# Kernel tuning notes

Hardware: AMD Instinct MI355X
Metric: run time of the kernel (lower is better)

The kernel has to match this reference:

```python
import jax, jax.numpy as jnp
import numpy as np

N_NODES = 50000
N_EDGES = 640000
N_REL = 8
IN_DIM = 128
HID_DIM = 128
OUT_DIM = 64


def setup_inputs() -> dict:
    key = jax.random.key(0)
    ks = jax.random.split(key, 8)
    features = jax.random.normal(ks[0], (N_NODES, IN_DIM), dtype=jnp.float32)
    src = jax.random.randint(ks[1], (N_EDGES,), 0, N_NODES, dtype=jnp.int32)
    dst = jax.random.randint(ks[2], (N_EDGES,), 0, N_NODES, dtype=jnp.int32)
    edge_types = jax.random.randint(ks[3], (N_EDGES,), 0, N_REL, dtype=jnp.int32)
    s1 = 1.0 / np.sqrt(IN_DIM)
    s2 = 1.0 / np.sqrt(HID_DIM)
    W1 = jax.random.normal(ks[4], (N_REL, IN_DIM, HID_DIM), dtype=jnp.float32) * s1
    W1_self = jax.random.normal(ks[5], (IN_DIM, HID_DIM), dtype=jnp.float32) * s1
    b1 = jnp.zeros((HID_DIM,), dtype=jnp.float32)
    W2 = jax.random.normal(ks[6], (N_REL, HID_DIM, OUT_DIM), dtype=jnp.float32) * s2
    W2_self = jax.random.normal(ks[7], (HID_DIM, OUT_DIM), dtype=jnp.float32) * s2
    b2 = jnp.zeros((OUT_DIM,), dtype=jnp.float32)
    return {"features": features, "src": src, "dst": dst, "edge_types": edge_types,
            "W1": W1, "W1_self": W1_self, "b1": b1,
            "W2": W2, "W2_self": W2_self, "b2": b2}


def _rel_graph_conv(h, src, dst, edge_types, W, W_self, b):
    # Precompute relation-specific transforms for all nodes: [R, N, Dout]
    rel = jnp.einsum('nd,rdo->rno', h, W)
    # Gather per-edge message W[etype(e)] @ h[src(e)]: [E, Dout]
    msg = rel[edge_types, src]
    # Scatter-sum to destination nodes
    agg = jax.ops.segment_sum(msg, dst, num_segments=h.shape[0])
    # Self-loop + bias (DGL RelGraphConv defaults: self_loop=True, bias=True)
    return agg + h @ W_self + b


def reference(features, src, dst, edge_types, W1, W1_self, b1, W2, W2_self, b2):
    h = jax.nn.relu(_rel_graph_conv(features, src, dst, edge_types, W1, W1_self, b1))
    logits = _rel_graph_conv(h, src, dst, edge_types, W2, W2_self, b2)
    return logits
```

## Files before the change

kernel.cpp:

```cpp
#include <hip/hip_runtime.h>
#include <hip/hip_bf16.h>
#include <stdint.h>

#define NN 50000
#define NE 640000
#define NR 8
#define NB_SCAN ((NN + 1023) / 1024)

typedef short bf16x8 __attribute__((ext_vector_type(8)));
typedef float f32x4  __attribute__((ext_vector_type(4)));

__device__ __forceinline__ unsigned short f2bf(float f) {
    union { float f; unsigned u; } v; v.f = f;
    unsigned r = v.u + 0x7FFF + ((v.u >> 16) & 1);
    return (unsigned short)(r >> 16);
}
__device__ __forceinline__ float bf2f(unsigned short s) {
    union { unsigned u; float f; } v; v.u = ((unsigned)s) << 16; return v.f;
}

__global__ void hist_kernel(const int* __restrict__ dst, int* __restrict__ counts) {
    int e = blockIdx.x * 256 + threadIdx.x;
    if (e < NE) atomicAdd(&counts[dst[e]], 1);
}

__global__ __launch_bounds__(1024) void blocksum_kernel(const int* __restrict__ counts,
                                                        int* __restrict__ bsum) {
    __shared__ int ws[16];
    int i = blockIdx.x * 1024 + threadIdx.x;
    int v = (i < NN) ? counts[i] : 0;
    #pragma unroll
    for (int d = 32; d > 0; d >>= 1) v += __shfl_down(v, d, 64);
    int wid = threadIdx.x >> 6, lane = threadIdx.x & 63;
    if (lane == 0) ws[wid] = v;
    __syncthreads();
    if (threadIdx.x < 16) {
        int s = ws[threadIdx.x];
        #pragma unroll
        for (int d = 8; d > 0; d >>= 1) s += __shfl_down(s, d, 16);
        if (threadIdx.x == 0) bsum[blockIdx.x] = s;
    }
}

__global__ __launch_bounds__(64) void scanbase_kernel(const int* __restrict__ bsum,
                                                      int* __restrict__ base,
                                                      int* __restrict__ offsets) {
    int lane = threadIdx.x;
    int v = (lane < NB_SCAN) ? bsum[lane] : 0;
    int incl = v;
    #pragma unroll
    for (int d = 1; d < 64; d <<= 1) {
        int n = __shfl_up(incl, d, 64);
        if (lane >= d) incl += n;
    }
    if (lane < NB_SCAN) base[lane] = incl - v;
    if (lane == 63) offsets[NN] = incl;
}

__global__ __launch_bounds__(1024) void scanlocal_kernel(const int* __restrict__ counts,
                                                         const int* __restrict__ base,
                                                         int* __restrict__ offsets,
                                                         int* __restrict__ cursor) {
    __shared__ int ws[16];
    __shared__ int wbase[16];
    int t = threadIdx.x;
    int i = blockIdx.x * 1024 + t;
    int v = (i < NN) ? counts[i] : 0;
    int lane = t & 63, wid = t >> 6;
    int incl = v;
    #pragma unroll
    for (int d = 1; d < 64; d <<= 1) {
        int n = __shfl_up(incl, d, 64);
        if (lane >= d) incl += n;
    }
    if (lane == 63) ws[wid] = incl;
    __syncthreads();
    if (t < 16) {
        int s = ws[t];
        int si = s;
        #pragma unroll
        for (int d = 1; d < 16; d <<= 1) {
            int n = __shfl_up(si, d, 16);
            if (t >= d) si += n;
        }
        wbase[t] = si - s;
    }
    __syncthreads();
    if (i < NN) {
        int excl = base[blockIdx.x] + wbase[wid] + incl - v;
        offsets[i] = excl;
        cursor[i]  = excl;
    }
}

__global__ void fill_kernel(const int* __restrict__ src, const int* __restrict__ dst,
                            const int* __restrict__ et, int* __restrict__ cursor,
                            int* __restrict__ rows) {
    int e = blockIdx.x * 256 + threadIdx.x;
    if (e < NE) {
        int pos = atomicAdd(&cursor[dst[e]], 1);
        rows[pos] = et[e] * NN + src[e];
    }
}

__global__ void cvt_bf16_kernel(const float* __restrict__ in, unsigned short* __restrict__ outp,
                                int n8) {
    int i = blockIdx.x * 256 + threadIdx.x;
    if (i >= n8) return;
    const float4* pp = (const float4*)in + (size_t)i * 2;
    float4 a = pp[0], b = pp[1];
    uint4 o;
    o.x = (unsigned)f2bf(a.x) | ((unsigned)f2bf(a.y) << 16);
    o.y = (unsigned)f2bf(a.z) | ((unsigned)f2bf(a.w) << 16);
    o.z = (unsigned)f2bf(b.x) | ((unsigned)f2bf(b.y) << 16);
    o.w = (unsigned)f2bf(b.z) | ((unsigned)f2bf(b.w) << 16);
    ((uint4*)outp)[i] = o;
}

template<int DOUTV>
__global__ void prepW_kernel(const float* __restrict__ W, const float* __restrict__ Wself,
                             unsigned short* __restrict__ WT) {
    int idx = blockIdx.x * 256 + threadIdx.x;
    if (idx >= 9 * DOUTV * 128) return;
    int k = idx & 127;
    int c = idx >> 7;
    int r = c / DOUTV;
    int o = c - r * DOUTV;
    float v = (r < 8) ? W[((size_t)r * 128 + k) * DOUTV + o]
                      : Wself[(size_t)k * DOUTV + o];
    WT[idx] = f2bf(v);
}

template<int BN, int BM>
__global__ __launch_bounds__(256) void mfma_gemm_kernel(
        const unsigned short* __restrict__ A,
        const unsigned short* __restrict__ WT,
        const float*  __restrict__ bias,
        unsigned short* __restrict__ relout,
        float*  __restrict__ selfout,
        int M) {
    __shared__ unsigned short Xs[BM * 128];
    __shared__ unsigned short Ws[BN * 128];
    const int t  = threadIdx.x;
    const int mb = blockIdx.x;
    const int bn = blockIdx.y;

    #pragma unroll
    for (int i = 0; i < BM / 16; i++) {
        int g = t + i * 256;
        int row = g >> 4, c = g & 15;
        int m = mb * BM + row;
        float4 v = make_float4(0.f, 0.f, 0.f, 0.f);
        if (m < M) v = *(const float4*)(A + (size_t)m * 128 + c * 8);
        *(float4*)((char*)Xs + row * 256 + ((c ^ (row & 15)) << 4)) = v;
    }
    #pragma unroll
    for (int i = 0; i < BN / 16; i++) {
        int g = t + i * 256;
        int row = g >> 4, c = g & 15;
        float4 v = *(const float4*)(WT + ((size_t)bn * BN + row) * 128 + c * 8);
        *(float4*)((char*)Ws + row * 256 + ((c ^ (row & 15)) << 4)) = v;
    }
    __syncthreads();

    const int lane = t & 63;
    const int w    = t >> 6;
    const int wm   = (BN == 128) ? (w & 1) * 64 : w * 64;
    const int wn   = (BN == 128) ? (w >> 1) * 64 : 0;
    const int r15  = lane & 15;
    const int q    = lane >> 4;

    f32x4 acc[4][4] = {};
    #pragma unroll
    for (int ks = 0; ks < 4; ks++) {
        bf16x8 af[4], bfr[4];
        int c = (ks * 4 + q) ^ r15;
        #pragma unroll
        for (int i = 0; i < 4; i++) {
            int row = wm + i * 16 + r15;
            af[i] = *(const bf16x8*)((const char*)Xs + row * 256 + (c << 4));
        }
        #pragma unroll
        for (int j = 0; j < 4; j++) {
            int row = wn + j * 16 + r15;
            bfr[j] = *(const bf16x8*)((const char*)Ws + row * 256 + (c << 4));
        }
        #pragma unroll
        for (int i = 0; i < 4; i++)
            #pragma unroll
            for (int j = 0; j < 4; j++)
                acc[i][j] = __builtin_amdgcn_mfma_f32_16x16x32_bf16(af[i], bfr[j], acc[i][j], 0, 0, 0);
    }

    const int rowq = q * 4;
    if (bn < 8) {
        unsigned short* O = relout + (size_t)bn * M * BN;
        #pragma unroll
        for (int i = 0; i < 4; i++) {
            #pragma unroll
            for (int reg = 0; reg < 4; reg++) {
                int m = mb * BM + wm + i * 16 + rowq + reg;
                if (m < M) {
                    #pragma unroll
                    for (int j = 0; j < 4; j++) {
                        int n = wn + j * 16 + r15;
                        O[(size_t)m * BN + n] = f2bf(acc[i][j][reg]);
                    }
                }
            }
        }
    } else {
        #pragma unroll
        for (int j = 0; j < 4; j++) {
            float bv = bias[wn + j * 16 + r15];
            #pragma unroll
            for (int i = 0; i < 4; i++) {
                #pragma unroll
                for (int reg = 0; reg < 4; reg++) {
                    int m = mb * BM + wm + i * 16 + rowq + reg;
                    if (m < M)
                        selfout[(size_t)m * BN + wn + j * 16 + r15] = acc[i][j][reg] + bv;
                }
            }
        }
    }
}

template<int DIM, bool RELU, bool OUTBF16>
__global__ __launch_bounds__(64) void gather_kernel(
        const int* __restrict__ offsets, const int* __restrict__ rows,
        const unsigned short* __restrict__ rel, const float* __restrict__ selfin,
        void* __restrict__ outp) {
    int n = blockIdx.x;
    int t = threadIdx.x;
    int o0 = offsets[n], o1 = offsets[n + 1];
    if (DIM == 128) {
        float2 acc = *(const float2*)&selfin[(size_t)n * 128 + 2 * t];
        for (int j = o0; j < o1; j++) {
            size_t row = (size_t)rows[j];
            unsigned pv = *(const unsigned*)&rel[row * 128 + 2 * t];
            acc.x += bf2f((unsigned short)(pv & 0xffff));
            acc.y += bf2f((unsigned short)(pv >> 16));
        }
        if (RELU) { acc.x = fmaxf(acc.x, 0.f); acc.y = fmaxf(acc.y, 0.f); }
        if (OUTBF16) {
            unsigned pv = (unsigned)f2bf(acc.x) | ((unsigned)f2bf(acc.y) << 16);
            ((unsigned*)outp)[(size_t)n * 64 + t] = pv;
        } else {
            ((float2*)outp)[(size_t)n * 64 + t] = acc;
        }
    } else {
        float acc = selfin[(size_t)n * 64 + t];
        for (int j = o0; j < o1; j++)
            acc += bf2f(rel[(size_t)rows[j] * 64 + t]);
        if (RELU) acc = fmaxf(acc, 0.f);
        ((float*)outp)[(size_t)n * 64 + t] = acc;
    }
}

extern "C" void kernel_launch(void* const* d_in, const int* in_sizes, int n_in,
                              void* d_out, int out_size, void* d_ws, size_t ws_size,
                              hipStream_t stream) {
    const float* X   = (const float*)d_in[0];
    const int*   src = (const int*)d_in[1];
    const int*   dst = (const int*)d_in[2];
    const int*   et  = (const int*)d_in[3];
    const float* W1  = (const float*)d_in[4];
    const float* W1s = (const float*)d_in[5];
    const float* b1  = (const float*)d_in[6];
    const float* W2  = (const float*)d_in[7];
    const float* W2s = (const float*)d_in[8];
    const float* b2  = (const float*)d_in[9];
    float* out = (float*)d_out;

    char* p = (char*)d_ws;
    unsigned short* rel = (unsigned short*)p; p += (size_t)NR * NN * 128 * 2;
    float* hself = (float*)p;          p += (size_t)NN * 128 * 4;
    unsigned short* Xbf = (unsigned short*)p; p += (size_t)NN * 128 * 2;
    unsigned short* W1T = (unsigned short*)p; p += (size_t)9 * 128 * 128 * 2;
    unsigned short* W2T = (unsigned short*)p; p += (size_t)9 * 64 * 128 * 2;
    int* counts  = (int*)p; p += (size_t)NN * 4;
    int* offsets = (int*)p; p += (size_t)(NN + 4) * 4;
    int* cursor  = (int*)p; p += (size_t)NN * 4;
    int* rows    = (int*)p; p += (size_t)NE * 4;
    int* bsum    = (int*)p; p += 64 * 4;
    int* bbase   = (int*)p; p += 64 * 4;

    hipMemsetAsync(counts, 0, NN * sizeof(int), stream);
    hist_kernel<<<(NE + 255) / 256, 256, 0, stream>>>(dst, counts);
    blocksum_kernel<<<NB_SCAN, 1024, 0, stream>>>(counts, bsum);
    scanbase_kernel<<<1, 64, 0, stream>>>(bsum, bbase, offsets);
    scanlocal_kernel<<<NB_SCAN, 1024, 0, stream>>>(counts, bbase, offsets, cursor);
    fill_kernel<<<(NE + 255) / 256, 256, 0, stream>>>(src, dst, et, cursor, rows);

    cvt_bf16_kernel<<<(NN * 128 / 8 + 255) / 256, 256, 0, stream>>>(X, Xbf, NN * 128 / 8);
    prepW_kernel<128><<<(9 * 128 * 128 + 255) / 256, 256, 0, stream>>>(W1, W1s, W1T);
    prepW_kernel<64><<<(9 * 64 * 128 + 255) / 256, 256, 0, stream>>>(W2, W2s, W2T);

    mfma_gemm_kernel<128, 128><<<dim3((NN + 127) / 128, 9), 256, 0, stream>>>(
        Xbf, W1T, b1, rel, hself, NN);
    gather_kernel<128, true, true><<<NN, 64, 0, stream>>>(offsets, rows, rel, hself, Xbf);

    mfma_gemm_kernel<64, 256><<<dim3((NN + 255) / 256, 9), 256, 0, stream>>>(
        Xbf, W2T, b2, rel, out, NN);
    gather_kernel<64, false, false><<<NN, 64, 0, stream>>>(offsets, rows, rel, out, out);
}
```

Measured before the change: 347.5 us.

## Aggregate-then-transform with per-relation CSR and fused gather+MFMA layer kernel

Replaces the transform-then-gather scheme, which materialised eight relation-specific feature matrices per node, with aggregate-first: edges are sorted by (relation, destination). For each 64-node tile, the kernel scatter-adds bf16 source features into an fp32 LDS buffer with shared-memory atomics, converts the result to bf16, and multiplies by that relation's weight using MFMA, all inside a single fused kernel per layer. This removes the large bf16 relation intermediate and its write/read traffic, and merges the self-loop, bias and ReLU into the same kernel. In exchange it adds LDS atomics, weights read straight from global memory inside the MFMA loop, eight serialized relation passes with barriers per block, a larger scan over N*R counts, and extra bf16 rounding of the aggregated sums.

```diff
diff --git a/kernel.cpp b/kernel.cpp
--- a/kernel.cpp
+++ b/kernel.cpp
@@ -5,7 +5,8 @@
 #define NN 50000
 #define NE 640000
 #define NR 8
-#define NB_SCAN ((NN + 1023) / 1024)
+#define NK (NR * NN)
+#define NB2 ((NK + 1023) / 1024)
 
 typedef short bf16x8 __attribute__((ext_vector_type(8)));
 typedef float f32x4  __attribute__((ext_vector_type(4)));
@@ -15,20 +16,18 @@
     unsigned r = v.u + 0x7FFF + ((v.u >> 16) & 1);
     return (unsigned short)(r >> 16);
 }
-__device__ __forceinline__ float bf2f(unsigned short s) {
-    union { unsigned u; float f; } v; v.u = ((unsigned)s) << 16; return v.f;
-}
-
-__global__ void hist_kernel(const int* __restrict__ dst, int* __restrict__ counts) {
+
+__global__ void hist2_kernel(const int* __restrict__ dst, const int* __restrict__ et,
+                             int* __restrict__ counts) {
     int e = blockIdx.x * 256 + threadIdx.x;
-    if (e < NE) atomicAdd(&counts[dst[e]], 1);
+    if (e < NE) atomicAdd(&counts[et[e] * NN + dst[e]], 1);
 }
 
 __global__ __launch_bounds__(1024) void blocksum_kernel(const int* __restrict__ counts,
-                                                        int* __restrict__ bsum) {
+                                                        int* __restrict__ bsum, int n) {
     __shared__ int ws[16];
     int i = blockIdx.x * 1024 + threadIdx.x;
-    int v = (i < NN) ? counts[i] : 0;
+    int v = (i < n) ? counts[i] : 0;
     #pragma unroll
     for (int d = 32; d > 0; d >>= 1) v += __shfl_down(v, d, 64);
     int wid = threadIdx.x >> 6, lane = threadIdx.x & 63;
@@ -42,64 +41,78 @@
     }
 }
 
-__global__ __launch_bounds__(64) void scanbase_kernel(const int* __restrict__ bsum,
-                                                      int* __restrict__ base,
-                                                      int* __restrict__ offsets) {
-    int lane = threadIdx.x;
-    int v = (lane < NB_SCAN) ? bsum[lane] : 0;
+__global__ __launch_bounds__(512) void scanbase_kernel(const int* __restrict__ bsum,
+                                                       int* __restrict__ base,
+                                                       int* __restrict__ total, int nb) {
+    __shared__ int ws[8];
+    int t = threadIdx.x, lane = t & 63, wid = t >> 6;
+    int v = (t < nb) ? bsum[t] : 0;
     int incl = v;
     #pragma unroll
     for (int d = 1; d < 64; d <<= 1) {
-        int n = __shfl_up(incl, d, 64);
-        if (lane >= d) incl += n;
-    }
-    if (lane < NB_SCAN) base[lane] = incl - v;
-    if (lane == 63) offsets[NN] = incl;
+        int nv = __shfl_up(incl, d, 64);
+        if (lane >= d) incl += nv;
+    }
+    if (lane == 63) ws[wid] = incl;
+    __syncthreads();
+    if (t < 8) {
+        int s = ws[t], si = s;
+        #pragma unroll
+        for (int d = 1; d < 8; d <<= 1) {
+            int nv = __shfl_up(si, d, 64);
+            if (t >= d) si += nv;
+        }
+        ws[t] = si - s;
+    }
+    __syncthreads();
+    int excl = ws[wid] + incl - v;
+    if (t < nb) base[t] = excl;
+    if (t == 511) total[0] = ws[7] + incl;
 }
 
 __global__ __launch_bounds__(1024) void scanlocal_kernel(const int* __restrict__ counts,
                                                          const int* __restrict__ base,
                                                          int* __restrict__ offsets,
-                                                         int* __restrict__ cursor) {
+                                                         int* __restrict__ cursor, int n) {
     __shared__ int ws[16];
     __shared__ int wbase[16];
     int t = threadIdx.x;
     int i = blockIdx.x * 1024 + t;
-    int v = (i < NN) ? counts[i] : 0;
+    int v = (i < n) ? counts[i] : 0;
     int lane = t & 63, wid = t >> 6;
     int incl = v;
     #pragma unroll
     for (int d = 1; d < 64; d <<= 1) {
-        int n = __shfl_up(incl, d, 64);
-        if (lane >= d) incl += n;
+        int nv = __shfl_up(incl, d, 64);
+        if (lane >= d) incl += nv;
     }
     if (lane == 63) ws[wid] = incl;
     __syncthreads();
     if (t < 16) {
-        int s = ws[t];
-        int si = s;
+        int s = ws[t], si = s;
         #pragma unroll
         for (int d = 1; d < 16; d <<= 1) {
-            int n = __shfl_up(si, d, 16);
-            if (t >= d) si += n;
+            int nv = __shfl_up(si, d, 16);
+            if (t >= d) si += nv;
         }
         wbase[t] = si - s;
     }
     __syncthreads();
-    if (i < NN) {
+    if (i < n) {
         int excl = base[blockIdx.x] + wbase[wid] + incl - v;
         offsets[i] = excl;
         cursor[i]  = excl;
     }
 }
 
-__global__ void fill_kernel(const int* __restrict__ src, const int* __restrict__ dst,
-                            const int* __restrict__ et, int* __restrict__ cursor,
-                            int* __restrict__ rows) {
+__global__ void fill2_kernel(const int* __restrict__ src, const int* __restrict__ dst,
+                             const int* __restrict__ et, int* __restrict__ cursor,
+                             int* __restrict__ esrc, int* __restrict__ edst) {
     int e = blockIdx.x * 256 + threadIdx.x;
     if (e < NE) {
-        int pos = atomicAdd(&cursor[dst[e]], 1);
-        rows[pos] = et[e] * NN + src[e];
+        int pos = atomicAdd(&cursor[et[e] * NN + dst[e]], 1);
+        esrc[pos] = src[e];
+        edst[pos] = dst[e];
     }
 }
 
@@ -131,130 +144,129 @@
     WT[idx] = f2bf(v);
 }
 
-template<int BN, int BM>
-__global__ __launch_bounds__(256) void mfma_gemm_kernel(
+template<int NOUT, bool RELU, bool OUTBF16>
+__global__ __launch_bounds__(256) void fused_layer(
         const unsigned short* __restrict__ A,
         const unsigned short* __restrict__ WT,
-        const float*  __restrict__ bias,
-        unsigned short* __restrict__ relout,
-        float*  __restrict__ selfout,
-        int M) {
-    __shared__ unsigned short Xs[BM * 128];
-    __shared__ unsigned short Ws[BN * 128];
-    const int t  = threadIdx.x;
-    const int mb = blockIdx.x;
-    const int bn = blockIdx.y;
-
-    #pragma unroll
-    for (int i = 0; i < BM / 16; i++) {
-        int g = t + i * 256;
+        const float* __restrict__ bias,
+        const int* __restrict__ off2,
+        const int* __restrict__ esrc,
+        const int* __restrict__ edst,
+        void* __restrict__ outp, int M) {
+    constexpr int CW = NOUT / 4;
+    constexpr int NJ = CW / 16;
+    __shared__ float Af[64 * 132];
+    __shared__ unsigned short Asw[64 * 128];
+
+    const int t = threadIdx.x;
+    const int n0 = blockIdx.x * 64;
+    const int bm = (M - n0 < 64) ? (M - n0) : 64;
+    const int lane = t & 63;
+    const int w = t >> 6;
+    const int r15 = lane & 15;
+    const int q = lane >> 4;
+
+    f32x4 acc[4][NJ] = {};
+
+    auto do_mfma = [&](int rr) {
+        #pragma unroll
+        for (int ks = 0; ks < 4; ks++) {
+            int c = (ks * 4 + q) ^ r15;
+            bf16x8 af[4];
+            #pragma unroll
+            for (int i = 0; i < 4; i++)
+                af[i] = *(const bf16x8*)((const char*)Asw + (i * 16 + r15) * 256 + (c << 4));
+            #pragma unroll
+            for (int j = 0; j < NJ; j++) {
+                bf16x8 bf = *(const bf16x8*)(WT +
+                    ((size_t)(rr * NOUT + w * CW + j * 16 + r15) << 7) + ks * 32 + q * 8);
+                #pragma unroll
+                for (int i = 0; i < 4; i++)
+                    acc[i][j] = __builtin_amdgcn_mfma_f32_16x16x32_bf16(af[i], bf, acc[i][j], 0, 0, 0);
+            }
+        }
+    };
+
+    #pragma unroll
+    for (int kk = 0; kk < 4; kk++) {
+        int g = t + kk * 256;
         int row = g >> 4, c = g & 15;
-        int m = mb * BM + row;
-        float4 v = make_float4(0.f, 0.f, 0.f, 0.f);
-        if (m < M) v = *(const float4*)(A + (size_t)m * 128 + c * 8);
-        *(float4*)((char*)Xs + row * 256 + ((c ^ (row & 15)) << 4)) = v;
-    }
-    #pragma unroll
-    for (int i = 0; i < BN / 16; i++) {
-        int g = t + i * 256;
-        int row = g >> 4, c = g & 15;
-        float4 v = *(const float4*)(WT + ((size_t)bn * BN + row) * 128 + c * 8);
-        *(float4*)((char*)Ws + row * 256 + ((c ^ (row & 15)) << 4)) = v;
-    }
-    __syncthreads();
-
-    const int lane = t & 63;
-    const int w    = t >> 6;
-    const int wm   = (BN == 128) ? (w & 1) * 64 : w * 64;
-    const int wn   = (BN == 128) ? (w >> 1) * 64 : 0;
-    const int r15  = lane & 15;
-    const int q    = lane >> 4;
-
-    f32x4 acc[4][4] = {};
-    #pragma unroll
-    for (int ks = 0; ks < 4; ks++) {
-        bf16x8 af[4], bfr[4];
-        int c = (ks * 4 + q) ^ r15;
+        uint4 v = make_uint4(0, 0, 0, 0);
+        if (row < bm) v = *(const uint4*)(A + ((size_t)(n0 + row) << 7) + c * 8);
+        *(uint4*)((char*)Asw + row * 256 + ((c ^ (row & 15)) << 4)) = v;
+    }
+    __syncthreads();
+    do_mfma(8);
+
+    for (int r = 0; r < 8; r++) {
+        #pragma unroll
+        for (int z = 0; z < 9; z++) {
+            int s4 = t + z * 256;
+            if (s4 < 2112) ((float4*)Af)[s4] = make_float4(0.f, 0.f, 0.f, 0.f);
+        }
+        __syncthreads();
+
+        int e0 = off2[r * NN + n0];
+        int e1 = off2[r * NN + n0 + bm];
+        for (int eb = e0 + w * 4; eb < e1; eb += 16) {
+            int ne = e1 - eb; ne = (ne > 4) ? 4 : ne;
+            int ss[4], dd[4];
+            #pragma unroll
+            for (int i = 0; i < 4; i++)
+                if (i < ne) { ss[i] = esrc[eb + i]; dd[i] = edst[eb + i] - n0; }
+            unsigned vv[4];
+            #pragma unroll
+            for (int i = 0; i < 4; i++)
+                if (i < ne) vv[i] = ((const unsigned*)A)[((size_t)ss[i] << 6) + lane];
+            #pragma unroll
+            for (int i = 0; i < 4; i++)
+                if (i < ne) {
+                    atomicAdd(&Af[dd[i] * 132 + lane],      __uint_as_float(vv[i] << 16));
+                    atomicAdd(&Af[dd[i] * 132 + 66 + lane], __uint_as_float(vv[i] & 0xffff0000u));
+                }
+        }
+        __syncthreads();
+
+        #pragma unroll
+        for (int kk = 0; kk < 4; kk++) {
+            int g = t + kk * 256;
+            int row = g >> 4, cc = g & 15;
+            const float* rp = &Af[row * 132];
+            unsigned short tmp[8];
+            #pragma unroll
+            for (int j = 0; j < 8; j++)
+                tmp[j] = f2bf(rp[(j & 1) * 66 + cc * 4 + (j >> 1)]);
+            uint4 pv;
+            pv.x = (unsigned)tmp[0] | ((unsigned)tmp[1] << 16);
+            pv.y = (unsigned)tmp[2] | ((unsigned)tmp[3] << 16);
+            pv.z = (unsigned)tmp[4] | ((unsigned)tmp[5] << 16);
+            pv.w = (unsigned)tmp[6] | ((unsigned)tmp[7] << 16);
+            *(uint4*)((char*)Asw + row * 256 + ((cc ^ (row & 15)) << 4)) = pv;
+        }
+        __syncthreads();
+
+        do_mfma(r);
+    }
+
+    #pragma unroll
+    for (int j = 0; j < NJ; j++) {
+        int col = w * CW + j * 16 + r15;
+        float bv = bias[col];
         #pragma unroll
         for (int i = 0; i < 4; i++) {
-            int row = wm + i * 16 + r15;
-            af[i] = *(const bf16x8*)((const char*)Xs + row * 256 + (c << 4));
-        }
-        #pragma unroll
-        for (int j = 0; j < 4; j++) {
-            int row = wn + j * 16 + r15;
-            bfr[j] = *(const bf16x8*)((const char*)Ws + row * 256 + (c << 4));
-        }
-        #pragma unroll
-        for (int i = 0; i < 4; i++)
-            #pragma unroll
-            for (int j = 0; j < 4; j++)
-                acc[i][j] = __builtin_amdgcn_mfma_f32_16x16x32_bf16(af[i], bfr[j], acc[i][j], 0, 0, 0);
-    }
-
-    const int rowq = q * 4;
-    if (bn < 8) {
-        unsigned short* O = relout + (size_t)bn * M * BN;
-        #pragma unroll
-        for (int i = 0; i < 4; i++) {
             #pragma unroll
             for (int reg = 0; reg < 4; reg++) {
-                int m = mb * BM + wm + i * 16 + rowq + reg;
+                int m = n0 + i * 16 + q * 4 + reg;
                 if (m < M) {
-                    #pragma unroll
-                    for (int j = 0; j < 4; j++) {
-                        int n = wn + j * 16 + r15;
-                        O[(size_t)m * BN + n] = f2bf(acc[i][j][reg]);
-                    }
+                    float v = acc[i][j][reg] + bv;
+                    if (RELU) v = fmaxf(v, 0.f);
+                    if (OUTBF16)
+                        ((unsigned short*)outp)[(size_t)m * NOUT + col] = f2bf(v);
+                    else
+                        ((float*)outp)[(size_t)m * NOUT + col] = v;
                 }
             }
         }
-    } else {
-        #pragma unroll
-        for (int j = 0; j < 4; j++) {
-            float bv = bias[wn + j * 16 + r15];
-            #pragma unroll
-            for (int i = 0; i < 4; i++) {
-                #pragma unroll
-                for (int reg = 0; reg < 4; reg++) {
-                    int m = mb * BM + wm + i * 16 + rowq + reg;
-                    if (m < M)
-                        selfout[(size_t)m * BN + wn + j * 16 + r15] = acc[i][j][reg] + bv;
-                }
-            }
-        }
-    }
-}
-
-template<int DIM, bool RELU, bool OUTBF16>
-__global__ __launch_bounds__(64) void gather_kernel(
-        const int* __restrict__ offsets, const int* __restrict__ rows,
-        const unsigned short* __restrict__ rel, const float* __restrict__ selfin,
-        void* __restrict__ outp) {
-    int n = blockIdx.x;
-    int t = threadIdx.x;
-    int o0 = offsets[n], o1 = offsets[n + 1];
-    if (DIM == 128) {
-        float2 acc = *(const float2*)&selfin[(size_t)n * 128 + 2 * t];
-        for (int j = o0; j < o1; j++) {
-            size_t row = (size_t)rows[j];
-            unsigned pv = *(const unsigned*)&rel[row * 128 + 2 * t];
-            acc.x += bf2f((unsigned short)(pv & 0xffff));
-            acc.y += bf2f((unsigned short)(pv >> 16));
-        }
-        if (RELU) { acc.x = fmaxf(acc.x, 0.f); acc.y = fmaxf(acc.y, 0.f); }
-        if (OUTBF16) {
-            unsigned pv = (unsigned)f2bf(acc.x) | ((unsigned)f2bf(acc.y) << 16);
-            ((unsigned*)outp)[(size_t)n * 64 + t] = pv;
-        } else {
-            ((float2*)outp)[(size_t)n * 64 + t] = acc;
-        }
-    } else {
-        float acc = selfin[(size_t)n * 64 + t];
-        for (int j = o0; j < o1; j++)
-            acc += bf2f(rel[(size_t)rows[j] * 64 + t]);
-        if (RELU) acc = fmaxf(acc, 0.f);
-        ((float*)outp)[(size_t)n * 64 + t] = acc;
     }
 }
 
@@ -274,34 +286,33 @@
     float* out = (float*)d_out;
 
     char* p = (char*)d_ws;
-    unsigned short* rel = (unsigned short*)p; p += (size_t)NR * NN * 128 * 2;
-    float* hself = (float*)p;          p += (size_t)NN * 128 * 4;
     unsigned short* Xbf = (unsigned short*)p; p += (size_t)NN * 128 * 2;
+    unsigned short* hbf = (unsigned short*)p; p += (size_t)NN * 128 * 2;
     unsigned short* W1T = (unsigned short*)p; p += (size_t)9 * 128 * 128 * 2;
     unsigned short* W2T = (unsigned short*)p; p += (size_t)9 * 64 * 128 * 2;
-    int* counts  = (int*)p; p += (size_t)NN * 4;
-    int* offsets = (int*)p; p += (size_t)(NN + 4) * 4;
-    int* cursor  = (int*)p; p += (size_t)NN * 4;
-    int* rows    = (int*)p; p += (size_t)NE * 4;
-    int* bsum    = (int*)p; p += 64 * 4;
-    int* bbase   = (int*)p; p += 64 * 4;
-
-    hipMemsetAsync(counts, 0, NN * sizeof(int), stream);
-    hist_kernel<<<(NE + 255) / 256, 256, 0, stream>>>(dst, counts);
-    blocksum_kernel<<<NB_SCAN, 1024, 0, stream>>>(counts, bsum);
-    scanbase_kernel<<<1, 64, 0, stream>>>(bsum, bbase, offsets);
-    scanlocal_kernel<<<NB_SCAN, 1024, 0, stream>>>(counts, bbase, offsets, cursor);
-    fill_kernel<<<(NE + 255) / 256, 256, 0, stream>>>(src, dst, et, cursor, rows);
+    int* counts2 = (int*)p; p += (size_t)NK * 4;
+    int* off2    = (int*)p; p += (size_t)(NK + 4) * 4;
+    int* cursor2 = (int*)p; p += (size_t)NK * 4;
+    int* esrc    = (int*)p; p += (size_t)NE * 4;
+    int* edst    = (int*)p; p += (size_t)NE * 4;
+    int* bsum    = (int*)p; p += 512 * 4;
+    int* bbase   = (int*)p; p += 512 * 4;
+
+    hipMemsetAsync(counts2, 0, (size_t)NK * sizeof(int), stream);
+    hist2_kernel<<<(NE + 255) / 256, 256, 0, stream>>>(dst, et, counts2);
+    blocksum_kernel<<<NB2, 1024, 0, stream>>>(counts2, bsum, NK);
+    scanbase_kernel<<<1, 512, 0, stream>>>(bsum, bbase, &off2[NK], NB2);
+    scanlocal_kernel<<<NB2, 1024, 0, stream>>>(counts2, bbase, off2, cursor2, NK);
+    fill2_kernel<<<(NE + 255) / 256, 256, 0, stream>>>(src, dst, et, cursor2, esrc, edst);
 
     cvt_bf16_kernel<<<(NN * 128 / 8 + 255) / 256, 256, 0, stream>>>(X, Xbf, NN * 128 / 8);
     prepW_kernel<128><<<(9 * 128 * 128 + 255) / 256, 256, 0, stream>>>(W1, W1s, W1T);
     prepW_kernel<64><<<(9 * 64 * 128 + 255) / 256, 256, 0, stream>>>(W2, W2s, W2T);
 
-    mfma_gemm_kernel<128, 128><<<dim3((NN + 127) / 128, 9), 256, 0, stream>>>(
-        Xbf, W1T, b1, rel, hself, NN);
-    gather_kernel<128, true, true><<<NN, 64, 0, stream>>>(offsets, rows, rel, hself, Xbf);
-
-    mfma_gemm_kernel<64, 256><<<dim3((NN + 255) / 256, 9), 256, 0, stream>>>(
-        Xbf, W2T, b2, rel, out, NN);
-    gather_kernel<64, false, false><<<NN, 64, 0, stream>>>(offsets, rows, rel, out, out);
-}
+    const int nblk = (NN + 63) / 64;
+
+    fused_layer<128, true, true><<<nblk, 256, 0, stream>>>(
+        Xbf, W1T, b1, off2, esrc, edst, hbf, NN);
+    fused_layer<64, false, false><<<nblk, 256, 0, stream>>>(
+        hbf, W2T, b2, off2, esrc, edst, out, NN);
+}
```

After: 1.331 ms. 283% more time.

## Read GEMM weights directly from global, pack gathers four nodes per block

Applied to the files above, without the earlier changes.

The GEMM no longer stages the weight tile in shared memory. Each wave loads its B fragments straight from global or L2, which halves LDS use and may raise occupancy, and layer 2 now uses 128-row tiles. The gather kernels process four destination nodes per 256-thread block and unroll the edge loop by four, so more row loads are in flight. The scan base kernel is generalised to 512 threads, which adds some overhead in exchange for flexibility.

```diff
diff --git a/kernel.cpp b/kernel.cpp
--- a/kernel.cpp
+++ b/kernel.cpp
@@ -5,7 +5,7 @@
 #define NN 50000
 #define NE 640000
 #define NR 8
-#define NB_SCAN ((NN + 1023) / 1024)
+#define NB1 ((NN + 1023) / 1024)
 
 typedef short bf16x8 __attribute__((ext_vector_type(8)));
 typedef float f32x4  __attribute__((ext_vector_type(4)));
@@ -25,10 +25,10 @@
 }
 
 __global__ __launch_bounds__(1024) void blocksum_kernel(const int* __restrict__ counts,
-                                                        int* __restrict__ bsum) {
+                                                        int* __restrict__ bsum, int n) {
     __shared__ int ws[16];
     int i = blockIdx.x * 1024 + threadIdx.x;
-    int v = (i < NN) ? counts[i] : 0;
+    int v = (i < n) ? counts[i] : 0;
     #pragma unroll
     for (int d = 32; d > 0; d >>= 1) v += __shfl_down(v, d, 64);
     int wid = threadIdx.x >> 6, lane = threadIdx.x & 63;
@@ -42,51 +42,64 @@
     }
 }
 
-__global__ __launch_bounds__(64) void scanbase_kernel(const int* __restrict__ bsum,
-                                                      int* __restrict__ base,
-                                                      int* __restrict__ offsets) {
-    int lane = threadIdx.x;
-    int v = (lane < NB_SCAN) ? bsum[lane] : 0;
+__global__ __launch_bounds__(512) void scanbase_kernel(const int* __restrict__ bsum,
+                                                       int* __restrict__ base,
+                                                       int* __restrict__ total, int nb) {
+    __shared__ int ws[8];
+    int t = threadIdx.x, lane = t & 63, wid = t >> 6;
+    int v = (t < nb) ? bsum[t] : 0;
     int incl = v;
     #pragma unroll
     for (int d = 1; d < 64; d <<= 1) {
-        int n = __shfl_up(incl, d, 64);
-        if (lane >= d) incl += n;
-    }
-    if (lane < NB_SCAN) base[lane] = incl - v;
-    if (lane == 63) offsets[NN] = incl;
+        int nv = __shfl_up(incl, d, 64);
+        if (lane >= d) incl += nv;
+    }
+    if (lane == 63) ws[wid] = incl;
+    __syncthreads();
+    if (t < 8) {
+        int s = ws[t], si = s;
+        #pragma unroll
+        for (int d = 1; d < 8; d <<= 1) {
+            int nv = __shfl_up(si, d, 64);
+            if (t >= d) si += nv;
+        }
+        ws[t] = si - s;
+    }
+    __syncthreads();
+    int excl = ws[wid] + incl - v;
+    if (t < nb) base[t] = excl;
+    if (t == 511) total[0] = ws[7] + incl;
 }
 
 __global__ __launch_bounds__(1024) void scanlocal_kernel(const int* __restrict__ counts,
                                                          const int* __restrict__ base,
                                                          int* __restrict__ offsets,
-                                                         int* __restrict__ cursor) {
+                                                         int* __restrict__ cursor, int n) {
     __shared__ int ws[16];
     __shared__ int wbase[16];
     int t = threadIdx.x;
     int i = blockIdx.x * 1024 + t;
-    int v = (i < NN) ? counts[i] : 0;
+    int v = (i < n) ? counts[i] : 0;
     int lane = t & 63, wid = t >> 6;
     int incl = v;
     #pragma unroll
     for (int d = 1; d < 64; d <<= 1) {
-        int n = __shfl_up(incl, d, 64);
-        if (lane >= d) incl += n;
+        int nv = __shfl_up(incl, d, 64);
+        if (lane >= d) incl += nv;
     }
     if (lane == 63) ws[wid] = incl;
     __syncthreads();
     if (t < 16) {
-        int s = ws[t];
-        int si = s;
+        int s = ws[t], si = s;
         #pragma unroll
         for (int d = 1; d < 16; d <<= 1) {
-            int n = __shfl_up(si, d, 16);
-            if (t >= d) si += n;
+            int nv = __shfl_up(si, d, 16);
+            if (t >= d) si += nv;
         }
         wbase[t] = si - s;
     }
     __syncthreads();
-    if (i < NN) {
+    if (i < n) {
         int excl = base[blockIdx.x] + wbase[wid] + incl - v;
         offsets[i] = excl;
         cursor[i]  = excl;
@@ -131,131 +144,138 @@
     WT[idx] = f2bf(v);
 }
 
-template<int BN, int BM>
-__global__ __launch_bounds__(256) void mfma_gemm_kernel(
+template<int NOUT>
+__global__ __launch_bounds__(256) void gemm_split(
         const unsigned short* __restrict__ A,
         const unsigned short* __restrict__ WT,
         const float*  __restrict__ bias,
         unsigned short* __restrict__ relout,
         float*  __restrict__ selfout,
         int M) {
-    __shared__ unsigned short Xs[BM * 128];
-    __shared__ unsigned short Ws[BN * 128];
+    constexpr int NJ = NOUT / 32;
+    __shared__ unsigned short Xs[128 * 128];
     const int t  = threadIdx.x;
     const int mb = blockIdx.x;
     const int bn = blockIdx.y;
 
     #pragma unroll
-    for (int i = 0; i < BM / 16; i++) {
+    for (int i = 0; i < 8; i++) {
         int g = t + i * 256;
         int row = g >> 4, c = g & 15;
-        int m = mb * BM + row;
-        float4 v = make_float4(0.f, 0.f, 0.f, 0.f);
-        if (m < M) v = *(const float4*)(A + (size_t)m * 128 + c * 8);
-        *(float4*)((char*)Xs + row * 256 + ((c ^ (row & 15)) << 4)) = v;
-    }
-    #pragma unroll
-    for (int i = 0; i < BN / 16; i++) {
-        int g = t + i * 256;
-        int row = g >> 4, c = g & 15;
-        float4 v = *(const float4*)(WT + ((size_t)bn * BN + row) * 128 + c * 8);
-        *(float4*)((char*)Ws + row * 256 + ((c ^ (row & 15)) << 4)) = v;
+        int m = mb * 128 + row;
+        uint4 v = make_uint4(0, 0, 0, 0);
+        if (m < M) v = *(const uint4*)(A + ((size_t)m << 7) + c * 8);
+        *(uint4*)((char*)Xs + row * 256 + ((c ^ (row & 15)) << 4)) = v;
     }
     __syncthreads();
 
     const int lane = t & 63;
     const int w    = t >> 6;
-    const int wm   = (BN == 128) ? (w & 1) * 64 : w * 64;
-    const int wn   = (BN == 128) ? (w >> 1) * 64 : 0;
+    const int wm   = (w & 1) * 64;
+    const int wn   = (w >> 1) * (NOUT / 2);
     const int r15  = lane & 15;
     const int q    = lane >> 4;
 
-    f32x4 acc[4][4] = {};
+    f32x4 acc[4][NJ] = {};
     #pragma unroll
     for (int ks = 0; ks < 4; ks++) {
-        bf16x8 af[4], bfr[4];
         int c = (ks * 4 + q) ^ r15;
-        #pragma unroll
-        for (int i = 0; i < 4; i++) {
-            int row = wm + i * 16 + r15;
-            af[i] = *(const bf16x8*)((const char*)Xs + row * 256 + (c << 4));
-        }
-        #pragma unroll
-        for (int j = 0; j < 4; j++) {
-            int row = wn + j * 16 + r15;
-            bfr[j] = *(const bf16x8*)((const char*)Ws + row * 256 + (c << 4));
-        }
+        bf16x8 af[4];
         #pragma unroll
         for (int i = 0; i < 4; i++)
+            af[i] = *(const bf16x8*)((const char*)Xs + (wm + i * 16 + r15) * 256 + (c << 4));
+        #pragma unroll
+        for (int j = 0; j < NJ; j++) {
+            bf16x8 bf = *(const bf16x8*)(WT +
+                ((size_t)(bn * NOUT + wn + j * 16 + r15) << 7) + ks * 32 + q * 8);
             #pragma unroll
-            for (int j = 0; j < 4; j++)
-                acc[i][j] = __builtin_amdgcn_mfma_f32_16x16x32_bf16(af[i], bfr[j], acc[i][j], 0, 0, 0);
+            for (int i = 0; i < 4; i++)
+                acc[i][j] = __builtin_amdgcn_mfma_f32_16x16x32_bf16(af[i], bf, acc[i][j], 0, 0, 0);
+        }
     }
 
     const int rowq = q * 4;
     if (bn < 8) {
-        unsigned short* O = relout + (size_t)bn * M * BN;
+        unsigned short* O = relout + (size_t)bn * M * NOUT;
         #pragma unroll
         for (int i = 0; i < 4; i++) {
             #pragma unroll
             for (int reg = 0; reg < 4; reg++) {
-                int m = mb * BM + wm + i * 16 + rowq + reg;
+                int m = mb * 128 + wm + i * 16 + rowq + reg;
                 if (m < M) {
                     #pragma unroll
-                    for (int j = 0; j < 4; j++) {
-                        int n = wn + j * 16 + r15;
-                        O[(size_t)m * BN + n] = f2bf(acc[i][j][reg]);
-                    }
+                    for (int j = 0; j < NJ; j++)
+                        O[(size_t)m * NOUT + wn + j * 16 + r15] = f2bf(acc[i][j][reg]);
                 }
             }
         }
     } else {
         #pragma unroll
-        for (int j = 0; j < 4; j++) {
+        for (int j = 0; j < NJ; j++) {
             float bv = bias[wn + j * 16 + r15];
             #pragma unroll
             for (int i = 0; i < 4; i++) {
                 #pragma unroll
                 for (int reg = 0; reg < 4; reg++) {
-                    int m = mb * BM + wm + i * 16 + rowq + reg;
+                    int m = mb * 128 + wm + i * 16 + rowq + reg;
                     if (m < M)
-                        selfout[(size_t)m * BN + wn + j * 16 + r15] = acc[i][j][reg] + bv;
+                        selfout[(size_t)m * NOUT + wn + j * 16 + r15] = acc[i][j][reg] + bv;
                 }
             }
         }
     }
 }
 
-template<int DIM, bool RELU, bool OUTBF16>
-__global__ __launch_bounds__(64) void gather_kernel(
+__global__ __launch_bounds__(256) void gather128(
         const int* __restrict__ offsets, const int* __restrict__ rows,
-        const unsigned short* __restrict__ rel, const float* __restrict__ selfin,
-        void* __restrict__ outp) {
-    int n = blockIdx.x;
-    int t = threadIdx.x;
+        const unsigned short* __restrict__ rel, const float* __restrict__ hself,
+        unsigned short* __restrict__ hbf) {
+    int wv = threadIdx.x >> 6, l = threadIdx.x & 63;
+    int n = blockIdx.x * 4 + wv;
     int o0 = offsets[n], o1 = offsets[n + 1];
-    if (DIM == 128) {
-        float2 acc = *(const float2*)&selfin[(size_t)n * 128 + 2 * t];
-        for (int j = o0; j < o1; j++) {
-            size_t row = (size_t)rows[j];
-            unsigned pv = *(const unsigned*)&rel[row * 128 + 2 * t];
-            acc.x += bf2f((unsigned short)(pv & 0xffff));
-            acc.y += bf2f((unsigned short)(pv >> 16));
-        }
-        if (RELU) { acc.x = fmaxf(acc.x, 0.f); acc.y = fmaxf(acc.y, 0.f); }
-        if (OUTBF16) {
-            unsigned pv = (unsigned)f2bf(acc.x) | ((unsigned)f2bf(acc.y) << 16);
-            ((unsigned*)outp)[(size_t)n * 64 + t] = pv;
-        } else {
-            ((float2*)outp)[(size_t)n * 64 + t] = acc;
-        }
-    } else {
-        float acc = selfin[(size_t)n * 64 + t];
-        for (int j = o0; j < o1; j++)
-            acc += bf2f(rel[(size_t)rows[j] * 64 + t]);
-        if (RELU) acc = fmaxf(acc, 0.f);
-        ((float*)outp)[(size_t)n * 64 + t] = acc;
-    }
+    float2 acc = *(const float2*)&hself[((size_t)n << 7) + 2 * l];
+    const unsigned* R = (const unsigned*)rel;
+    int j = o0;
+    for (; j + 4 <= o1; j += 4) {
+        int r0 = rows[j], r1 = rows[j + 1], r2 = rows[j + 2], r3 = rows[j + 3];
+        unsigned p0 = R[((size_t)r0 << 6) + l];
+        unsigned p1 = R[((size_t)r1 << 6) + l];
+        unsigned p2 = R[((size_t)r2 << 6) + l];
+        unsigned p3 = R[((size_t)r3 << 6) + l];
+        acc.x += __uint_as_float(p0 << 16) + __uint_as_float(p1 << 16)
+               + __uint_as_float(p2 << 16) + __uint_as_float(p3 << 16);
+        acc.y += __uint_as_float(p0 & 0xffff0000u) + __uint_as_float(p1 & 0xffff0000u)
+               + __uint_as_float(p2 & 0xffff0000u) + __uint_as_float(p3 & 0xffff0000u);
+    }
+    for (; j < o1; ++j) {
+        unsigned p = R[((size_t)rows[j] << 6) + l];
+        acc.x += __uint_as_float(p << 16);
+        acc.y += __uint_as_float(p & 0xffff0000u);
+    }
+    acc.x = fmaxf(acc.x, 0.f);
+    acc.y = fmaxf(acc.y, 0.f);
+    ((unsigned*)hbf)[((size_t)n << 6) + l] = (unsigned)f2bf(acc.x) | ((unsigned)f2bf(acc.y) << 16);
+}
+
+__global__ __launch_bounds__(256) void gather64(
+        const int* __restrict__ offsets, const int* __restrict__ rows,
+        const unsigned short* __restrict__ rel, float* __restrict__ io) {
+    int wv = threadIdx.x >> 6, l = threadIdx.x & 63;
+    int n = blockIdx.x * 4 + wv;
+    int o0 = offsets[n], o1 = offsets[n + 1];
+    float acc = io[((size_t)n << 6) + l];
+    int j = o0;
+    for (; j + 4 <= o1; j += 4) {
+        int r0 = rows[j], r1 = rows[j + 1], r2 = rows[j + 2], r3 = rows[j + 3];
+        unsigned short v0 = rel[((size_t)r0 << 6) + l];
+        unsigned short v1 = rel[((size_t)r1 << 6) + l];
+        unsigned short v2 = rel[((size_t)r2 << 6) + l];
+        unsigned short v3 = rel[((size_t)r3 << 6) + l];
+        acc += bf2f(v0) + bf2f(v1) + bf2f(v2) + bf2f(v3);
+    }
+    for (; j < o1; ++j)
+        acc += bf2f(rel[((size_t)rows[j] << 6) + l]);
+    io[((size_t)n << 6) + l] = acc;
 }
 
 extern "C" void kernel_launch(void* const* d_in, const int* in_sizes, int n_in,
@@ -283,25 +303,26 @@
     int* offsets = (int*)p; p += (size_t)(NN + 4) * 4;
     int* cursor  = (int*)p; p += (size_t)NN * 4;
     int* rows    = (int*)p; p += (size_t)NE * 4;
-    int* bsum    = (int*)p; p += 64 * 4;
-    int* bbase   = (int*)p; p += 64 * 4;
+    int* bsum    = (int*)p; p += 512 * 4;
+    int* bbase   = (int*)p; p += 512 * 4;
 
     hipMemsetAsync(counts, 0, NN * sizeof(int), stream);
     hist_kernel<<<(NE + 255) / 256, 256, 0, stream>>>(dst, counts);
-    blocksum_kernel<<<NB_SCAN, 1024, 0, stream>>>(counts, bsum);
-    scanbase_kernel<<<1, 64, 0, stream>>>(bsum, bbase, offsets);
-    scanlocal_kernel<<<NB_SCAN, 1024, 0, stream>>>(counts, bbase, offsets, cursor);
+    blocksum_kernel<<<NB1, 1024, 0, stream>>>(counts, bsum, NN);
+    scanbase_kernel<<<1, 512, 0, stream>>>(bsum, bbase, &offsets[NN], NB1);
+    scanlocal_kernel<<<NB1, 1024, 0, stream>>>(counts, bbase, offsets, cursor, NN);
     fill_kernel<<<(NE + 255) / 256, 256, 0, stream>>>(src, dst, et, cursor, rows);
 
     cvt_bf16_kernel<<<(NN * 128 / 8 + 255) / 256, 256, 0, stream>>>(X, Xbf, NN * 128 / 8);
     prepW_kernel<128><<<(9 * 128 * 128 + 255) / 256, 256, 0, stream>>>(W1, W1s, W1T);
     prepW_kernel<64><<<(9 * 64 * 128 + 255) / 256, 256, 0, stream>>>(W2, W2s, W2T);
 
-    mfma_gemm_kernel<128, 128><<<dim3((NN + 127) / 128, 9), 256, 0, stream>>>(
-        Xbf, W1T, b1, rel, hself, NN);
-    gather_kernel<128, true, true><<<NN, 64, 0, stream>>>(offsets, rows, rel, hself, Xbf);
-
-    mfma_gemm_kernel<64, 256><<<dim3((NN + 255) / 256, 9), 256, 0, stream>>>(
-        Xbf, W2T, b2, rel, out, NN);
-    gather_kernel<64, false, false><<<NN, 64, 0, stream>>>(offsets, rows, rel, out, out);
-}
+    const int mblocks = (NN + 127) / 128;
+    const int gblocks = NN / 4;
+
+    gemm_split<128><<<dim3(mblocks, 9), 256, 0, stream>>>(Xbf, W1T, b1, rel, hself, NN);
+    gather128<<<gblocks, 256, 0, stream>>>(offsets, rows, rel, hself, Xbf);
+
+    gemm_split<64><<<dim3(mblocks, 9), 256, 0, stream>>>(Xbf, W2T, b2, rel, out, NN);
+    gather64<<<gblocks, 256, 0, stream>>>(offsets, rows, rel, out);
+}
```

Result: no change. 344.1 us (-1.0%).
